# Kernel optimization log

Hardware: AMD Instinct MI355X
Metric: run time of the kernel (lower is better)

## Reference

```python
import jax, jax.numpy as jnp
import numpy as np

BATCH = 8192
EMBED_DIM = 256
INPUT_DIM = 3 * EMBED_DIM  # 768
NUM_LAYERS = 4
VOCAB_SIZES = [100000, 100000, 1000]
EPS = 1e-5


def setup_inputs() -> dict:
    key = jax.random.key(0)
    ks = jax.random.split(key, 20)
    inp = {}
    inp["x_p"] = jax.random.randint(ks[0], (BATCH,), 0, VOCAB_SIZES[0])
    inp["x_a"] = jax.random.randint(ks[1], (BATCH,), 0, VOCAB_SIZES[1])
    inp["x_c"] = jax.random.randint(ks[2], (BATCH,), 0, VOCAB_SIZES[2])
    inp["y_true"] = jax.random.uniform(ks[3], (BATCH, 1), dtype=jnp.float32)
    # embedding tables (nn.Embedding default init N(0,1))
    inp["E0"] = jax.random.normal(ks[4], (VOCAB_SIZES[0], EMBED_DIM), dtype=jnp.float32)
    inp["E1"] = jax.random.normal(ks[5], (VOCAB_SIZES[1], EMBED_DIM), dtype=jnp.float32)
    inp["E2"] = jax.random.normal(ks[6], (VOCAB_SIZES[2], EMBED_DIM), dtype=jnp.float32)
    lim = 1.0 / np.sqrt(INPUT_DIM)
    inp["Wd"] = jax.random.uniform(ks[7], (NUM_LAYERS, INPUT_DIM, INPUT_DIM), jnp.float32, -lim, lim)
    inp["bd"] = jnp.zeros((NUM_LAYERS, INPUT_DIM), jnp.float32)
    inp["Ws"] = jax.random.uniform(ks[8], (NUM_LAYERS, INPUT_DIM, INPUT_DIM), jnp.float32, -lim, lim)
    inp["bs"] = jnp.zeros((NUM_LAYERS, INPUT_DIM), jnp.float32)
    inp["wfd"] = jax.random.uniform(ks[9], (INPUT_DIM,), jnp.float32, -lim, lim)
    inp["bfd"] = jax.random.uniform(ks[10], (), jnp.float32, -lim, lim)
    inp["wfs"] = jax.random.uniform(ks[11], (INPUT_DIM,), jnp.float32, -lim, lim)
    inp["bfs"] = jax.random.uniform(ks[12], (), jnp.float32, -lim, lim)
    return inp


def _cross_network(x, W, b, net_id, mask_key):
    # per layer: cross = x @ W[l].T + b[l]; mask = bernoulli(sigmoid(layernorm over FULL tensor)); x += cross*mask
    for l in range(NUM_LAYERS):
        cross = jnp.einsum("bd,od->bo", x, W[l]) + b[l]
        m = jnp.mean(cross)
        v = jnp.mean(jnp.square(cross - m))  # F.layer_norm(x, x.size()): normalize over all elements
        ln = (cross - m) * jax.lax.rsqrt(v + EPS)
        p = jax.nn.sigmoid(ln)
        k = jax.random.fold_in(mask_key, net_id * NUM_LAYERS + l)
        mask = jax.random.bernoulli(k, p).astype(x.dtype)
        x = x + cross * mask
    return x


def _bce(p, y):
    return jnp.mean(-(y * jnp.log(p) + (1.0 - y) * jnp.log(1.0 - p)))


def reference(x_p, x_a, x_c, y_true, E0, E1, E2, Wd, bd, Ws, bs, wfd, bfd, wfs, bfs):
    h = EMBED_DIM // 2
    e0, e1, e2 = E0[x_p], E1[x_a], E2[x_c]  # [B, embed_dim] each
    e_a = jnp.concatenate([e0[:, :h], e1[:, :h], e2[:, :h]], axis=-1)
    e_b = jnp.concatenate([e0[:, h:], e1[:, h:], e2[:, h:]], axis=-1)
    x = jnp.concatenate([e_a, e_b], axis=-1)  # [B, 3*embed_dim]

    mask_key = jax.random.key(42)
    x_d = _cross_network(x, Wd, bd, 0, mask_key)
    x_s = _cross_network(x, Ws, bs, 1, mask_key)

    sd_d = jax.nn.sigmoid(x_d @ wfd + bfd)[:, None]  # fc_d(x_d)
    ss_s = jax.nn.sigmoid(x_s @ wfs + bfs)[:, None]  # fc_s(x_s)
    sd_s = jax.nn.sigmoid(x_s @ wfd + bfd)[:, None]  # fc_d(x_s)
    ss_d = jax.nn.sigmoid(x_d @ wfs + bfs)[:, None]  # fc_s(x_d)
    y_pred_d = 0.5 * (sd_d + ss_s)
    y_pred_s = 0.5 * (sd_s + ss_d)

    loss_d = _bce(y_pred_d, y_true)
    loss_s = _bce(y_pred_s, y_true)
    bce_loss = loss_d + loss_s
    weight_d = jnp.maximum(0.0, loss_d - bce_loss)
    weight_s = jnp.maximum(0.0, loss_s - bce_loss)
    tri_loss = bce_loss + weight_d * loss_d + weight_s * loss_s
    return (y_pred_d, tri_loss)
```

## Files before the change

kernel.cpp:

```cpp
#include <hip/hip_runtime.h>
#include <hip/hip_bf16.h>
#include <cstdint>
#include <cstddef>

#define BATCH   8192
#define DIM     768
#define NTOT    6291456
#define NLAYERS 4

typedef _Float16 half8 __attribute__((ext_vector_type(8)));
typedef float    f32x4 __attribute__((ext_vector_type(4)));

#define AS_GLOBAL __attribute__((address_space(1)))
#define AS_LDS    __attribute__((address_space(3)))

__device__ __forceinline__ void async_copy16(const void* g, void* l) {
  __builtin_amdgcn_global_load_lds((AS_GLOBAL const uint32_t*)g,
                                   (AS_LDS uint32_t*)l, 16, 0, 0);
}

__host__ __device__ __forceinline__ uint32_t rotl32(uint32_t v, int d) {
  return (v << d) | (v >> (32 - d));
}

__host__ __device__ __forceinline__ void threefry2x32(
    uint32_t k0, uint32_t k1, uint32_t x0, uint32_t x1,
    uint32_t& o0, uint32_t& o1) {
  uint32_t ks2 = k0 ^ k1 ^ 0x1BD11BDAu;
  x0 += k0; x1 += k1;
#define TF_R(r) { x0 += x1; x1 = rotl32(x1, (r)) ^ x0; }
  TF_R(13) TF_R(15) TF_R(26) TF_R(6)
  x0 += k1; x1 += ks2 + 1u;
  TF_R(17) TF_R(29) TF_R(16) TF_R(24)
  x0 += ks2; x1 += k0 + 2u;
  TF_R(13) TF_R(15) TF_R(26) TF_R(6)
  x0 += k0; x1 += k1 + 3u;
  TF_R(17) TF_R(29) TF_R(16) TF_R(24)
  x0 += k1; x1 += ks2 + 4u;
  TF_R(13) TF_R(15) TF_R(26) TF_R(6)
  x0 += ks2; x1 += k0 + 5u;
#undef TF_R
  o0 = x0; o1 = x1;
}

__device__ __forceinline__ double sigmoid_d(double x) {
  return 1.0 / (1.0 + exp(-x));
}

__global__ __launch_bounds__(256) void gather_kernel(
    const int* __restrict__ x_p, const int* __restrict__ x_a,
    const int* __restrict__ x_c,
    const float* __restrict__ E0, const float* __restrict__ E1,
    const float* __restrict__ E2,
    _Float16* __restrict__ xdh, _Float16* __restrict__ xdl,
    _Float16* __restrict__ xsh, _Float16* __restrict__ xsl) {
  int j = blockIdx.x * 256 + threadIdx.x;
  int b = j / DIM;
  int f = j - b * DIM;
  int half_ = f / 384;
  int w = f - half_ * 384;
  int t = w >> 7;
  int c = (w & 127) + (half_ << 7);
  int idx;
  const float* E;
  if (t == 0)      { E = E0; idx = x_p[b]; }
  else if (t == 1) { E = E1; idx = x_a[b]; }
  else             { E = E2; idx = x_c[b]; }
  float v = E[(size_t)idx * 256 + c];
  _Float16 h = (_Float16)v;
  _Float16 l = (_Float16)(v - (float)h);
  xdh[j] = h; xdl[j] = l;
  xsh[j] = h; xsl[j] = l;
}

__global__ __launch_bounds__(256) void split_w_kernel(
    const float* __restrict__ Wd, const float* __restrict__ Ws,
    _Float16* __restrict__ Wh, _Float16* __restrict__ Wl) {
  int idx = blockIdx.x * 256 + threadIdx.x;
  const int perNet = NLAYERS * DIM * DIM;
  float v = (idx < perNet) ? Wd[idx] : Ws[idx - perNet];
  _Float16 h = (_Float16)v;
  Wh[idx] = h;
  Wl[idx] = (_Float16)(v - (float)h);
}

__global__ __launch_bounds__(256, 3) void gemm_mfma_kernel(
    const _Float16* __restrict__ xdh, const _Float16* __restrict__ xdl,
    const _Float16* __restrict__ xsh, const _Float16* __restrict__ xsl,
    const _Float16* __restrict__ Wh, const _Float16* __restrict__ Wl,
    const float* __restrict__ bd, const float* __restrict__ bs,
    float* __restrict__ crd, float* __restrict__ crs,
    double* __restrict__ partials, int layer) {
  const int net = blockIdx.z;
  const float* bias = (net ? bs : bd) + layer * DIM;
  float* C = net ? crs : crd;

  const int wave = threadIdx.x >> 6, lane = threadIdx.x & 63;
  const int quad = lane >> 4, l16 = lane & 15;
  const int m0 = blockIdx.x * 128;
  const int n0 = blockIdx.y * 128;

  __shared__ _Float16 lds[4 * 5120];

  const _Float16* gbase;
  int rowbase;
  switch (wave) {
    case 0:  gbase = net ? xsh : xdh; rowbase = m0; break;
    case 1:  gbase = net ? xsl : xdl; rowbase = m0; break;
    case 2:  gbase = Wh + ((size_t)net * NLAYERS + layer) * DIM * DIM; rowbase = n0; break;
    default: gbase = Wl + ((size_t)net * NLAYERS + layer) * DIM * DIM; rowbase = n0; break;
  }
  int soff[10];
#pragma unroll
  for (int j = 0; j < 10; ++j) {
    int s  = j * 64 + lane;
    int r  = (s * 52429) >> 18;
    int kk = (s - 5 * r) & 3;
    soff[j] = (rowbase + r) * DIM + kk * 8;
  }
  _Float16* ldsw = &lds[wave * 5120];

  const int wm = (wave >> 1) * 64, wn = (wave & 1) * 64;
  const int fslotA = ((wm + l16) * 5 + quad) * 8;
  const int fslotB = ((wn + l16) * 5 + quad) * 8;

  f32x4 acc[4][4];
#pragma unroll
  for (int i = 0; i < 4; ++i)
#pragma unroll
    for (int j = 0; j < 4; ++j) acc[i][j] = (f32x4){0.f, 0.f, 0.f, 0.f};

  for (int k0 = 0; k0 < DIM; k0 += 32) {
    __syncthreads();
#pragma unroll
    for (int j = 0; j < 10; ++j)
      async_copy16(gbase + soff[j] + k0, ldsw + j * 512);
    __syncthreads();

    half8 ah[4], al[4], bh[4], bl[4];
#pragma unroll
    for (int t = 0; t < 4; ++t) {
      ah[t] = *(const half8*)&lds[        fslotA + t * 640];
      al[t] = *(const half8*)&lds[ 5120 + fslotA + t * 640];
      bh[t] = *(const half8*)&lds[10240 + fslotB + t * 640];
      bl[t] = *(const half8*)&lds[15360 + fslotB + t * 640];
    }
#pragma unroll
    for (int mt = 0; mt < 4; ++mt)
#pragma unroll
      for (int nt = 0; nt < 4; ++nt) {
        f32x4 a = acc[mt][nt];
        a = __builtin_amdgcn_mfma_f32_16x16x32_f16(ah[mt], bh[nt], a, 0, 0, 0);
        a = __builtin_amdgcn_mfma_f32_16x16x32_f16(al[mt], bh[nt], a, 0, 0, 0);
        a = __builtin_amdgcn_mfma_f32_16x16x32_f16(ah[mt], bl[nt], a, 0, 0, 0);
        acc[mt][nt] = a;
      }
  }

  float biasv[4];
#pragma unroll
  for (int nt = 0; nt < 4; ++nt) biasv[nt] = bias[n0 + wn + nt * 16 + l16];

  double s = 0.0, q = 0.0;
#pragma unroll
  for (int mt = 0; mt < 4; ++mt) {
#pragma unroll
    for (int nt = 0; nt < 4; ++nt) {
      int n = n0 + wn + nt * 16 + l16;
#pragma unroll
      for (int r = 0; r < 4; ++r) {
        int m = m0 + wm + mt * 16 + quad * 4 + r;
        float v = acc[mt][nt][r] + biasv[nt];
        C[(size_t)m * DIM + n] = v;
        s += (double)v;
        q += (double)v * (double)v;
      }
    }
  }
#pragma unroll
  for (int off = 32; off > 0; off >>= 1) {
    s += __shfl_down(s, off);
    q += __shfl_down(q, off);
  }
  __shared__ double red[4][2];
  if (lane == 0) { red[wave][0] = s; red[wave][1] = q; }
  __syncthreads();
  if (threadIdx.x == 0) {
    double S = red[0][0] + red[1][0] + red[2][0] + red[3][0];
    double Q = red[0][1] + red[1][1] + red[2][1] + red[3][1];
    int bid = blockIdx.y * 64 + blockIdx.x;
    partials[((size_t)net * 384 + bid) * 2 + 0] = S;
    partials[((size_t)net * 384 + bid) * 2 + 1] = Q;
  }
}

__global__ __launch_bounds__(256) void finalize_stats_kernel(
    const double* __restrict__ partials, double* __restrict__ stats) {
  int net = blockIdx.x;
  const double* P = partials + (size_t)net * 384 * 2;
  int tid = threadIdx.x;
  double s = 0.0, q = 0.0;
  for (int i = tid; i < 384; i += 256) {
    s += P[i * 2 + 0];
    q += P[i * 2 + 1];
  }
#pragma unroll
  for (int off = 32; off > 0; off >>= 1) {
    s += __shfl_down(s, off);
    q += __shfl_down(q, off);
  }
  __shared__ double red[4][2];
  int wave = tid >> 6, lane = tid & 63;
  if (lane == 0) { red[wave][0] = s; red[wave][1] = q; }
  __syncthreads();
  if (tid == 0) {
    stats[net * 2 + 0] = red[0][0] + red[1][0] + red[2][0] + red[3][0];
    stats[net * 2 + 1] = red[0][1] + red[1][1] + red[2][1] + red[3][1];
  }
}

__global__ __launch_bounds__(256) void mask_update_kernel(
    _Float16* __restrict__ xdh, _Float16* __restrict__ xdl,
    _Float16* __restrict__ xsh, _Float16* __restrict__ xsl,
    const float* __restrict__ crd, const float* __restrict__ crs,
    const double* __restrict__ stats,
    uint32_t kd0, uint32_t kd1, uint32_t ks0, uint32_t ks1) {
  const int net = blockIdx.y;
  _Float16* xh = net ? xsh : xdh;
  _Float16* xl = net ? xsl : xdl;
  const float* cr = net ? crs : crd;
  const uint32_t k0 = net ? ks0 : kd0;
  const uint32_t k1 = net ? ks1 : kd1;

  const double invN = 1.0 / (double)NTOT;
  double meand = stats[net * 2 + 0] * invN;
  double vard  = stats[net * 2 + 1] * invN - meand * meand;
  float m  = (float)meand;
  float v  = (float)vard;
  float sv = v + 1e-5f;
  float rs = (float)(1.0 / sqrt((double)sv));

  uint32_t j = blockIdx.x * 256u + threadIdx.x;
  float c = cr[j];
  float ln = (c - m) * rs;
  float p = (float)sigmoid_d((double)ln);
  uint32_t o0, o1;
  threefry2x32(k0, k1, 0u, j, o0, o1);
  uint32_t bits = o0 ^ o1;
  float u = __uint_as_float(0x3F800000u | (bits >> 9)) - 1.0f;

  float xv = (float)xh[j] + (float)xl[j];
  if (u < p) xv += c;
  _Float16 h = (_Float16)xv;
  xh[j] = h;
  xl[j] = (_Float16)(xv - (float)h);
}

__global__ __launch_bounds__(256) void head_kernel(
    const _Float16* __restrict__ xdh, const _Float16* __restrict__ xdl,
    const _Float16* __restrict__ xsh, const _Float16* __restrict__ xsl,
    const float* __restrict__ wfd, const float* __restrict__ wfs,
    const float* __restrict__ bfd_p, const float* __restrict__ bfs_p,
    const float* __restrict__ y_true,
    float* __restrict__ out, double* __restrict__ bce_part) {
  const int wave = threadIdx.x >> 6;
  const int lane = threadIdx.x & 63;
  const int row = blockIdx.x * 4 + wave;
  const size_t base = (size_t)row * DIM;

  float dd = 0.f, dsw = 0.f, sd = 0.f, ssw = 0.f;
  for (int t = lane; t < DIM; t += 64) {
    float vd = (float)xdh[base + t] + (float)xdl[base + t];
    float vs = (float)xsh[base + t] + (float)xsl[base + t];
    float wd = wfd[t], ws = wfs[t];
    dd  = fmaf(vd, wd, dd);
    dsw = fmaf(vd, ws, dsw);
    sd  = fmaf(vs, wd, sd);
    ssw = fmaf(vs, ws, ssw);
  }
#pragma unroll
  for (int off = 32; off > 0; off >>= 1) {
    dd  += __shfl_down(dd, off);
    dsw += __shfl_down(dsw, off);
    sd  += __shfl_down(sd, off);
    ssw += __shfl_down(ssw, off);
  }
  __shared__ double redd[4], reds[4];
  if (lane == 0) {
    float bfd = *bfd_p, bfs = *bfs_p;
    double sdd = sigmoid_d((double)(dd + bfd));
    double ssd = sigmoid_d((double)(dsw + bfs));
    double sds = sigmoid_d((double)(sd + bfd));
    double sss = sigmoid_d((double)(ssw + bfs));
    double ypd = 0.5 * (sdd + sss);
    double yps = 0.5 * (sds + ssd);
    out[row] = (float)ypd;
    double y = (double)y_true[row];
    redd[wave] = -(y * log(ypd) + (1.0 - y) * log(1.0 - ypd));
    reds[wave] = -(y * log(yps) + (1.0 - y) * log(1.0 - yps));
  }
  __syncthreads();
  if (threadIdx.x == 0) {
    bce_part[(size_t)blockIdx.x * 2 + 0] = redd[0] + redd[1] + redd[2] + redd[3];
    bce_part[(size_t)blockIdx.x * 2 + 1] = reds[0] + reds[1] + reds[2] + reds[3];
  }
}

__global__ __launch_bounds__(256) void loss_kernel(
    const double* __restrict__ bce_part, float* __restrict__ out_tri) {
  int tid = threadIdx.x;
  double sdl = 0.0, ssl = 0.0;
  for (int i = tid; i < 2048; i += 256) {
    sdl += bce_part[i * 2 + 0];
    ssl += bce_part[i * 2 + 1];
  }
#pragma unroll
  for (int off = 32; off > 0; off >>= 1) {
    sdl += __shfl_down(sdl, off);
    ssl += __shfl_down(ssl, off);
  }
  __shared__ double red[4][2];
  int wave = tid >> 6, lane = tid & 63;
  if (lane == 0) { red[wave][0] = sdl; red[wave][1] = ssl; }
  __syncthreads();
  if (tid == 0) {
    double loss_d = (red[0][0] + red[1][0] + red[2][0] + red[3][0]) / (double)BATCH;
    double loss_s = (red[0][1] + red[1][1] + red[2][1] + red[3][1]) / (double)BATCH;
    double bce = loss_d + loss_s;
    double wd = fmax(0.0, loss_d - bce);
    double ws = fmax(0.0, loss_s - bce);
    out_tri[0] = (float)(bce + wd * loss_d + ws * loss_s);
  }
}

extern "C" void kernel_launch(void* const* d_in, const int* in_sizes, int n_in,
                              void* d_out, int out_size, void* d_ws, size_t ws_size,
                              hipStream_t stream) {
  const int* x_p = (const int*)d_in[0];
  const int* x_a = (const int*)d_in[1];
  const int* x_c = (const int*)d_in[2];
  const float* y_true = (const float*)d_in[3];
  const float* E0 = (const float*)d_in[4];
  const float* E1 = (const float*)d_in[5];
  const float* E2 = (const float*)d_in[6];
  const float* Wd = (const float*)d_in[7];
  const float* bd = (const float*)d_in[8];
  const float* Ws = (const float*)d_in[9];
  const float* bs = (const float*)d_in[10];
  const float* wfd = (const float*)d_in[11];
  const float* bfd = (const float*)d_in[12];
  const float* wfs = (const float*)d_in[13];
  const float* bfs = (const float*)d_in[14];
  float* out = (float*)d_out;

  char* p = (char*)d_ws;
  float* crd = (float*)p;                 p += (size_t)NTOT * 4;
  float* crs = (float*)p;                 p += (size_t)NTOT * 4;
  double* partials = (double*)p;          p += (size_t)2 * 384 * 2 * 8;
  double* stats    = (double*)p;          p += 4 * 8;
  double* bce_part = (double*)p;          p += (size_t)2048 * 2 * 8;
  _Float16* xdh = (_Float16*)p;           p += (size_t)NTOT * 2;
  _Float16* xdl = (_Float16*)p;           p += (size_t)NTOT * 2;
  _Float16* xsh = (_Float16*)p;           p += (size_t)NTOT * 2;
  _Float16* xsl = (_Float16*)p;           p += (size_t)NTOT * 2;
  _Float16* Wh  = (_Float16*)p;           p += (size_t)2 * NLAYERS * DIM * DIM * 2;
  _Float16* Wl  = (_Float16*)p;           p += (size_t)2 * NLAYERS * DIM * DIM * 2;

  gather_kernel<<<NTOT / 256, 256, 0, stream>>>(
      x_p, x_a, x_c, E0, E1, E2, xdh, xdl, xsh, xsl);
  split_w_kernel<<<2 * NLAYERS * DIM * DIM / 256, 256, 0, stream>>>(Wd, Ws, Wh, Wl);

  for (int l = 0; l < NLAYERS; ++l) {
    gemm_mfma_kernel<<<dim3(64, 6, 2), 256, 0, stream>>>(
        xdh, xdl, xsh, xsl, Wh, Wl, bd, bs, crd, crs, partials, l);
    finalize_stats_kernel<<<2, 256, 0, stream>>>(partials, stats);
    uint32_t kd0, kd1, ks0, ks1;
    threefry2x32(0u, 42u, 0u, (uint32_t)l, kd0, kd1);
    threefry2x32(0u, 42u, 0u, (uint32_t)(4 + l), ks0, ks1);
    mask_update_kernel<<<dim3(NTOT / 256, 2), 256, 0, stream>>>(
        xdh, xdl, xsh, xsl, crd, crs, stats, kd0, kd1, ks0, ks1);
  }

  head_kernel<<<BATCH / 4, 256, 0, stream>>>(
      xdh, xdl, xsh, xsl, wfd, wfs, bfd, bfs, y_true, out, bce_part);
  loss_kernel<<<1, 256, 0, stream>>>(bce_part, out + BATCH);
}
```

Measured before the change: 800.5 us.

## Double-buffer GEMM LDS tiles with XOR swizzle and add fast-path float sigmoid

The GEMM kernel now double-buffers its LDS tiles. The next k-slice's async global-to-LDS copies are issued before the current slice's MFMAs, which removes one barrier per iteration and lets loads overlap compute. The padded (stride 5) LDS layout is replaced by an XOR swizzle, and the occupancy hint drops from 3 to 2 blocks per CU because LDS use grows. The mask kernel computes the sigmoid in float with __expf and falls back to the double-precision sigmoid only when the random draw lies within 1e-4 of the probability, so the Bernoulli decisions stay exact while the double math is mostly avoided.

```diff
diff --git a/kernel.cpp b/kernel.cpp
--- a/kernel.cpp
+++ b/kernel.cpp
@@ -84,7 +84,7 @@
   Wl[idx] = (_Float16)(v - (float)h);
 }
 
-__global__ __launch_bounds__(256, 3) void gemm_mfma_kernel(
+__global__ __launch_bounds__(256, 2) void gemm_mfma_kernel(
     const _Float16* __restrict__ xdh, const _Float16* __restrict__ xdl,
     const _Float16* __restrict__ xsh, const _Float16* __restrict__ xsl,
     const _Float16* __restrict__ Wh, const _Float16* __restrict__ Wl,
@@ -100,7 +100,7 @@
   const int m0 = blockIdx.x * 128;
   const int n0 = blockIdx.y * 128;
 
-  __shared__ _Float16 lds[4 * 5120];
+  __shared__ _Float16 lds[2 * 4 * 4096];
 
   const _Float16* gbase;
   int rowbase;
@@ -110,19 +110,24 @@
     case 2:  gbase = Wh + ((size_t)net * NLAYERS + layer) * DIM * DIM; rowbase = n0; break;
     default: gbase = Wl + ((size_t)net * NLAYERS + layer) * DIM * DIM; rowbase = n0; break;
   }
-  int soff[10];
-#pragma unroll
-  for (int j = 0; j < 10; ++j) {
-    int s  = j * 64 + lane;
-    int r  = (s * 52429) >> 18;
-    int kk = (s - 5 * r) & 3;
-    soff[j] = (rowbase + r) * DIM + kk * 8;
-  }
-  _Float16* ldsw = &lds[wave * 5120];
+  int soff[8];
+#pragma unroll
+  for (int j = 0; j < 8; ++j) {
+    int s   = j * 64 + lane;
+    int row = s >> 2;
+    int kk  = (s & 3) ^ (row & 3);
+    soff[j] = (rowbase + row) * DIM + kk * 8;
+  }
+  const int wreg = wave * 4096;
 
   const int wm = (wave >> 1) * 64, wn = (wave & 1) * 64;
-  const int fslotA = ((wm + l16) * 5 + quad) * 8;
-  const int fslotB = ((wn + l16) * 5 + quad) * 8;
+  const int qx = quad ^ (l16 & 3);
+  int fA[4], fB[4];
+#pragma unroll
+  for (int t = 0; t < 4; ++t) {
+    fA[t] = ((wm + t * 16 + l16) * 4 + qx) * 8;
+    fB[t] = ((wn + t * 16 + l16) * 4 + qx) * 8;
+  }
 
   f32x4 acc[4][4];
 #pragma unroll
@@ -130,20 +135,27 @@
 #pragma unroll
     for (int j = 0; j < 4; ++j) acc[i][j] = (f32x4){0.f, 0.f, 0.f, 0.f};
 
+#pragma unroll
+  for (int j = 0; j < 8; ++j)
+    async_copy16(gbase + soff[j], &lds[wreg + j * 512]);
+
+  int buf = 0;
   for (int k0 = 0; k0 < DIM; k0 += 32) {
     __syncthreads();
-#pragma unroll
-    for (int j = 0; j < 10; ++j)
-      async_copy16(gbase + soff[j] + k0, ldsw + j * 512);
-    __syncthreads();
-
+    if (k0 + 32 < DIM) {
+      const int nb = (buf ^ 1) * 16384;
+#pragma unroll
+      for (int j = 0; j < 8; ++j)
+        async_copy16(gbase + soff[j] + (k0 + 32), &lds[nb + wreg + j * 512]);
+    }
+    const int cb = buf * 16384;
     half8 ah[4], al[4], bh[4], bl[4];
 #pragma unroll
     for (int t = 0; t < 4; ++t) {
-      ah[t] = *(const half8*)&lds[        fslotA + t * 640];
-      al[t] = *(const half8*)&lds[ 5120 + fslotA + t * 640];
-      bh[t] = *(const half8*)&lds[10240 + fslotB + t * 640];
-      bl[t] = *(const half8*)&lds[15360 + fslotB + t * 640];
+      ah[t] = *(const half8*)&lds[cb         + fA[t]];
+      al[t] = *(const half8*)&lds[cb +  4096 + fA[t]];
+      bh[t] = *(const half8*)&lds[cb +  8192 + fB[t]];
+      bl[t] = *(const half8*)&lds[cb + 12288 + fB[t]];
     }
 #pragma unroll
     for (int mt = 0; mt < 4; ++mt)
@@ -155,6 +167,7 @@
         a = __builtin_amdgcn_mfma_f32_16x16x32_f16(ah[mt], bl[nt], a, 0, 0, 0);
         acc[mt][nt] = a;
       }
+    buf ^= 1;
   }
 
   float biasv[4];
@@ -243,14 +256,23 @@
   uint32_t j = blockIdx.x * 256u + threadIdx.x;
   float c = cr[j];
   float ln = (c - m) * rs;
-  float p = (float)sigmoid_d((double)ln);
   uint32_t o0, o1;
   threefry2x32(k0, k1, 0u, j, o0, o1);
   uint32_t bits = o0 ^ o1;
   float u = __uint_as_float(0x3F800000u | (bits >> 9)) - 1.0f;
 
+  float pf = 1.0f / (1.0f + __expf(-ln));
+  bool take;
+  float diff = u - pf;
+  if (__builtin_expect(fabsf(diff) > 1e-4f, 1)) {
+    take = diff < 0.0f;
+  } else {
+    float pd = (float)sigmoid_d((double)ln);
+    take = u < pd;
+  }
+
   float xv = (float)xh[j] + (float)xl[j];
-  if (u < p) xv += c;
+  if (take) xv += c;
   _Float16 h = (_Float16)xv;
   xh[j] = h;
   xl[j] = (_Float16)(xv - (float)h);
```

Result: no change. 802.1 us (+0.2%).
